# Optimization experiments

Measured on AMD Instinct MI355X. Metric: run time of the kernel, lower is better.

The kernel has to match this reference:

```python
import jax, jax.numpy as jnp
import numpy as np

V, D, T_BLK, H, HS = 50257, 512, 2048, 8, 64
B, T = 2, 2048


def setup_inputs() -> dict:
    key = jax.random.key(0)
    ks = jax.random.split(key, 12)
    s = 0.02
    return {
        "idx": jax.random.randint(ks[0], (B, T), 0, V),
        "targets": jax.random.randint(ks[1], (B, T), 0, V),
        "tok_emb": jax.random.normal(ks[2], (V, D), jnp.float32) * s,
        "pos_emb": jax.random.normal(ks[3], (T_BLK, D), jnp.float32) * s,
        "wq": jax.random.normal(ks[4], (H, D, HS), jnp.float32) * s,
        "wk": jax.random.normal(ks[5], (H, D, HS), jnp.float32) * s,
        "wv": jax.random.normal(ks[6], (H, D, HS), jnp.float32) * s,
        "w1": jax.random.normal(ks[7], (D, D), jnp.float32) * s,
        "b1": jnp.zeros((D,), jnp.float32),
        "w_head": jax.random.normal(ks[8], (D, V), jnp.float32) * s,
        "b_head": jnp.zeros((V,), jnp.float32),
    }


def _forward(idx, targets, tok_emb, pos_emb, wq, wk, wv, w1, b1, w_head, b_head):
    b, t = idx.shape
    x = tok_emb[idx] + pos_emb[:t]                        # [B,T,D]
    # batched per-head QKV (equivalent to the per-head Linear loop)
    q = jnp.einsum("btd,hde->bhte", x, wq)                # [B,H,T,hs]
    k = jnp.einsum("btd,hde->bhte", x, wk)
    v = jnp.einsum("btd,hde->bhte", x, wv)
    scores = jnp.einsum("bhte,bhse->bhts", q, k) / jnp.sqrt(jnp.float32(HS))
    causal = jnp.tril(jnp.ones((t, t), bool))
    scores = jnp.where(causal, scores, -jnp.inf)
    weights = jax.nn.softmax(scores, axis=-1)
    att = jnp.einsum("bhts,bhse->bhte", weights, v)       # [B,H,T,hs]
    att = att.transpose(0, 2, 1, 3).reshape(b, t, H * HS)  # head-concat order
    x_ff = jax.nn.relu(att @ w1 + b1)                      # [B,T,D]
    logits = x_ff @ w_head + b_head                        # [B,T,V]
    logp = jax.nn.log_softmax(logits, axis=-1)
    loss = -jnp.mean(jnp.take_along_axis(logp, targets[..., None], axis=-1))
    return logits, loss


def reference(idx, targets, tok_emb, pos_emb, wq, wk, wv, w1, b1, w_head, b_head):
    return _forward(idx, targets, tok_emb, pos_emb, wq, wk, wv, w1, b1, w_head, b_head)
```

## Files before the change

kernel.cpp:

```cpp
#include <hip/hip_runtime.h>
#include <hip/hip_bf16.h>
#include <stdint.h>

#define V_SZ   50257
#define NPAD   50432
#define NT_HEAD 197
#define D_SZ   512
#define HS_SZ  64
#define H_N    8
#define T_SZ   2048
#define ROWS   4096

typedef __bf16 bf16x8 __attribute__((ext_vector_type(8)));
typedef __bf16 bf16x4 __attribute__((ext_vector_type(4)));
typedef float  f32x4  __attribute__((ext_vector_type(4)));

__device__ __forceinline__ void gload_lds16(const void* g, void* l) {
  auto gp = (const __attribute__((address_space(1))) uint32_t*)(uintptr_t)g;
  auto lp = (__attribute__((address_space(3))) uint32_t*)(uintptr_t)l;
  __builtin_amdgcn_global_load_lds(gp, lp, 16, 0, 0);
}

__global__ __launch_bounds__(256) void k_embed(const int* __restrict__ idx,
    const float* __restrict__ tok, const float* __restrict__ pos,
    __bf16* __restrict__ xb) {
  const int row = blockIdx.x;
  const int tpos = row & (T_SZ - 1);
  const int tokid = idx[row];
  const int d = threadIdx.x * 2;
  float2 tv = *(const float2*)(tok + (size_t)tokid * D_SZ + d);
  float2 pv = *(const float2*)(pos + (size_t)tpos * D_SZ + d);
  __bf16* o = xb + (size_t)row * D_SZ + d;
  o[0] = (__bf16)(tv.x + pv.x);
  o[1] = (__bf16)(tv.y + pv.y);
}

__global__ __launch_bounds__(256) void k_prep_wqkv(const float* __restrict__ wq,
    const float* __restrict__ wk, const float* __restrict__ wv, __bf16* __restrict__ dst) {
  const int id = blockIdx.x * 256 + threadIdx.x;
  const int n = id >> 9, dd = id & 511;
  const int mi = n >> 9, rem = n & 511, h = rem >> 6, e = rem & 63;
  const float* src = (mi == 0) ? wq : ((mi == 1) ? wk : wv);
  dst[id] = (__bf16)src[((size_t)h * D_SZ + dd) * HS_SZ + e];
}

__global__ __launch_bounds__(256) void k_prep_w1(const float* __restrict__ w1,
                                                 __bf16* __restrict__ dst) {
  const int id = blockIdx.x * 256 + threadIdx.x;
  const int n = id >> 9, kk = id & 511;
  dst[id] = (__bf16)w1[(size_t)kk * D_SZ + n];
}

__global__ void k_prep_wh(const float* __restrict__ wh, __bf16* __restrict__ dst) {
  __shared__ float tile[32][33];
  const int n0 = blockIdx.x * 32, d0 = blockIdx.y * 32;
  const int tx = threadIdx.x, ty = threadIdx.y;
  #pragma unroll
  for (int i = 0; i < 4; ++i) {
    int dd = d0 + ty + i * 8, n = n0 + tx;
    tile[ty + i * 8][tx] = (n < V_SZ) ? wh[(size_t)dd * V_SZ + n] : 0.f;
  }
  __syncthreads();
  #pragma unroll
  for (int i = 0; i < 4; ++i) {
    int n = n0 + ty + i * 8, dd = d0 + tx;
    dst[(size_t)n * D_SZ + dd] = (__bf16)tile[tx][ty + i * 8];
  }
}

template <int EPI>
__global__ __launch_bounds__(256) void k_gemm(const __bf16* __restrict__ A,
    const __bf16* __restrict__ Bt, const float* __restrict__ bias,
    __bf16* __restrict__ outH, __bf16* __restrict__ outK, __bf16* __restrict__ outV) {
  __shared__ __bf16 As[128 * 32];
  __shared__ __bf16 Bs[128 * 32];
  const int t = threadIdx.x, lane = t & 63, w = t >> 6;
  const int wr = w >> 1, wc = w & 1;
  const int m0 = blockIdx.x * 128, n0 = blockIdx.y * 128;
  const int srow = lane >> 2, k8 = (lane & 3) * 8;

  f32x4 zero = {0.f, 0.f, 0.f, 0.f};
  f32x4 acc[4][4];
  #pragma unroll
  for (int mm = 0; mm < 4; ++mm)
    #pragma unroll
    for (int nn = 0; nn < 4; ++nn) acc[mm][nn] = zero;

  const __bf16* Ag = A  + (size_t)(m0 + w * 16 + srow) * D_SZ + k8;
  const __bf16* Bg = Bt + (size_t)(n0 + w * 16 + srow) * D_SZ + k8;
  char* AsB = (char*)As + w * 1024;
  char* BsB = (char*)Bs + w * 1024;
  const int kslot = (lane >> 4) * 8;
  const int arow = wr * 64 + (lane & 15);
  const int brow = wc * 64 + (lane & 15);

  for (int kt = 0; kt < 16; ++kt) {
    const int k0 = kt * 32;
    gload_lds16(Ag + k0,             AsB);
    gload_lds16(Ag + 64 * D_SZ + k0, AsB + 4096);
    gload_lds16(Bg + k0,             BsB);
    gload_lds16(Bg + 64 * D_SZ + k0, BsB + 4096);
    __syncthreads();

    bf16x8 af[4], bfr[4];
    #pragma unroll
    for (int mm = 0; mm < 4; ++mm)
      af[mm] = *(const bf16x8*)(As + (arow + mm * 16) * 32 + kslot);
    #pragma unroll
    for (int nn = 0; nn < 4; ++nn)
      bfr[nn] = *(const bf16x8*)(Bs + (brow + nn * 16) * 32 + kslot);
    #pragma unroll
    for (int mm = 0; mm < 4; ++mm)
      #pragma unroll
      for (int nn = 0; nn < 4; ++nn)
        acc[mm][nn] = __builtin_amdgcn_mfma_f32_16x16x32_bf16(af[mm], bfr[nn], acc[mm][nn], 0, 0, 0);
    __syncthreads();
  }

  const int lrow = (lane >> 4) * 4, lcol = lane & 15;
  #pragma unroll
  for (int mm = 0; mm < 4; ++mm) {
    #pragma unroll
    for (int nn = 0; nn < 4; ++nn) {
      const int grow0 = m0 + wr * 64 + mm * 16 + lrow;
      const int gcol  = n0 + wc * 64 + nn * 16 + lcol;
      if (EPI == 0) {
        const int mi = gcol >> 9, rem = gcol & 511, hh = rem >> 6, e = rem & 63;
        const int bb = grow0 >> 11, tt0 = grow0 & 2047;
        const int bhh = bb * H_N + hh;
        if (mi == 2) {
          bf16x4 pk = { (__bf16)acc[mm][nn][0], (__bf16)acc[mm][nn][1],
                        (__bf16)acc[mm][nn][2], (__bf16)acc[mm][nn][3] };
          *(bf16x4*)(outV + ((size_t)bhh * HS_SZ + e) * T_SZ + tt0) = pk;
        } else {
          __bf16* dq = (mi == 0 ? outH : outK) + ((size_t)bhh * T_SZ + tt0) * HS_SZ + e;
          const float sc = (mi == 0) ? 0.125f : 1.f;
          #pragma unroll
          for (int j = 0; j < 4; ++j) dq[(size_t)j * HS_SZ] = (__bf16)(acc[mm][nn][j] * sc);
        }
      } else {
        #pragma unroll
        for (int j = 0; j < 4; ++j) {
          float xv = acc[mm][nn][j] + bias[gcol];
          outH[(size_t)(grow0 + j) * D_SZ + gcol] = (__bf16)(xv > 0.f ? xv : 0.f);
        }
      }
    }
  }
}

__global__ __launch_bounds__(512, 2) void k_ghead(const __bf16* __restrict__ A,
    const __bf16* __restrict__ Bt, const float* __restrict__ bias,
    float* __restrict__ logits, float2* __restrict__ part) {
  __shared__ char lds[131072];
  const int t = threadIdx.x, lane = t & 63, w = t >> 6;
  const int wr = w >> 2, wc = w & 3;
  const int m0 = blockIdx.x * 256, n0 = blockIdx.y * 256;
  const int r8 = lane >> 3, cc = lane & 7;
  const int lm = lane & 15, g = lane >> 4, l7 = lane & 7;
  const int csw = (cc ^ r8) << 4;
  const int srow8 = w * 8 + r8;

  f32x4 acc[8][4];
  #pragma unroll
  for (int mm = 0; mm < 8; ++mm)
    #pragma unroll
    for (int nn = 0; nn < 4; ++nn) acc[mm][nn] = f32x4{0.f, 0.f, 0.f, 0.f};

  const char* Ab = (const char*)A  + (size_t)m0 * (D_SZ * 2);
  const char* Bb = (const char*)Bt + (size_t)n0 * (D_SZ * 2);

  auto STAGE = [&](int buf, int kt) {
    char* Al = lds + buf * 65536;
    char* Bl = Al + 32768;
    const char* Asrc = Ab + kt * 128;
    const char* Bsrc = Bb + kt * 128;
    #pragma unroll
    for (int i = 0; i < 4; ++i) {
      gload_lds16(Asrc + (size_t)(i * 64 + srow8) * 1024 + csw, Al + (i * 64 + w * 8) * 128);
      gload_lds16(Bsrc + (size_t)(i * 64 + srow8) * 1024 + csw, Bl + (i * 64 + w * 8) * 128);
    }
  };

  STAGE(0, 0);
  STAGE(1, 1);
  asm volatile("s_waitcnt vmcnt(8)" ::: "memory");
  __builtin_amdgcn_s_barrier();
  asm volatile("" ::: "memory");

  for (int kt = 0; kt < 8; ++kt) {
    const char* Al = lds + (kt & 1) * 65536;
    const char* Bl = Al + 32768;
    #pragma unroll
    for (int kh = 0; kh < 2; ++kh) {
      const int ch = ((g + kh * 4) ^ l7) << 4;
      bf16x8 a[8], b[4];
      #pragma unroll
      for (int mm = 0; mm < 8; ++mm)
        a[mm] = *(const bf16x8*)(Al + (wr * 128 + mm * 16 + lm) * 128 + ch);
      #pragma unroll
      for (int nn = 0; nn < 4; ++nn)
        b[nn] = *(const bf16x8*)(Bl + (wc * 64 + nn * 16 + lm) * 128 + ch);
      #pragma unroll
      for (int mm = 0; mm < 8; ++mm)
        #pragma unroll
        for (int nn = 0; nn < 4; ++nn)
          acc[mm][nn] = __builtin_amdgcn_mfma_f32_16x16x32_bf16(a[mm], b[nn], acc[mm][nn], 0, 0, 0);
    }
    if (kt == 7) break;
    __builtin_amdgcn_s_barrier();
    asm volatile("" ::: "memory");
    if (kt < 6) {
      STAGE(kt & 1, kt + 2);
      asm volatile("s_waitcnt vmcnt(8)" ::: "memory");
    } else {
      asm volatile("s_waitcnt vmcnt(0)" ::: "memory");
    }
    __builtin_amdgcn_s_barrier();
    asm volatile("" ::: "memory");
  }
  __syncthreads();

  float* tr   = (float*)lds;
  float* redS = tr + 32 * 260;
  const int colL = wc * 64 + lm;
  float bj[4]; int vok[4];
  #pragma unroll
  for (int nn = 0; nn < 4; ++nn) {
    const int gc = n0 + colL + nn * 16;
    vok[nn] = (gc < V_SZ);
    bj[nn] = vok[nn] ? bias[gc] : 0.f;
  }
  const int r32s = t >> 4, c16 = t & 15;
  #pragma unroll
  for (int mm = 0; mm < 8; ++mm) {
    if (mm) __syncthreads();
    float sj[4];
    #pragma unroll
    for (int j = 0; j < 4; ++j) {
      const int r32 = wr * 16 + g * 4 + j;
      float s = 0.f;
      #pragma unroll
      for (int nn = 0; nn < 4; ++nn) {
        const float v = acc[mm][nn][j] + bj[nn];
        tr[r32 * 260 + colL + nn * 16] = v;
        if (vok[nn]) s += __expf(v);
      }
      sj[j] = s;
    }
    #pragma unroll
    for (int j = 0; j < 4; ++j) {
      float s = sj[j];
      s += __shfl_xor(s, 1); s += __shfl_xor(s, 2);
      s += __shfl_xor(s, 4); s += __shfl_xor(s, 8);
      if (lm == 0) redS[(wr * 128 + mm * 16 + g * 4 + j) * 4 + wc] = s;
    }
    __syncthreads();
    const int grow = m0 + (r32s >> 4) * 128 + mm * 16 + (r32s & 15);
    float* gp = logits + (size_t)grow * V_SZ;
    #pragma unroll
    for (int i = 0; i < 4; ++i) {
      const int c4 = c16 + 16 * i;
      const int gc0 = n0 + c4 * 4;
      f32x4 vv = *(const f32x4*)(tr + r32s * 260 + c4 * 4);
      if (gc0 + 3 < V_SZ) {
        __builtin_nontemporal_store(vv, (f32x4*)(gp + gc0));
      } else {
        if (gc0     < V_SZ) __builtin_nontemporal_store(vv.x, gp + gc0);
        if (gc0 + 1 < V_SZ) __builtin_nontemporal_store(vv.y, gp + gc0 + 1);
        if (gc0 + 2 < V_SZ) __builtin_nontemporal_store(vv.z, gp + gc0 + 2);
        if (gc0 + 3 < V_SZ) __builtin_nontemporal_store(vv.w, gp + gc0 + 3);
      }
    }
  }
  __syncthreads();
  if (t < 256) {
    const float S = redS[t * 4] + redS[t * 4 + 1] + redS[t * 4 + 2] + redS[t * 4 + 3];
    part[(size_t)(m0 + t) * NT_HEAD + blockIdx.y] = float2{0.f, S};
  }
}

__global__ __launch_bounds__(256) void k_attn(const __bf16* __restrict__ qbf,
    const __bf16* __restrict__ kbf, const __bf16* __restrict__ vbf,
    __bf16* __restrict__ xatt) {
  const int qt = 31 - blockIdx.x;
  const int bh = blockIdx.y;
  const int b = bh >> 3, h = bh & 7;
  const int t = threadIdx.x, lane = t & 63, w = t >> 6;
  const int qr = lane & 15, g = lane >> 4, r7 = qr & 7;
  __shared__ __bf16 Klds[64 * 64];
  __shared__ __bf16 Vt[64 * 64];
  __shared__ __bf16 Plds[4][16 * 72];

  const int qglob = qt * 64 + w * 16 + qr;
  const __bf16* qrow_g = qbf + ((size_t)bh * T_SZ + qglob) * HS_SZ + g * 8;
  const bf16x8 qf0 = *(const bf16x8*)(qrow_g);
  const bf16x8 qf1 = *(const bf16x8*)(qrow_g + 32);

  f32x4 att[4];
  #pragma unroll
  for (int n = 0; n < 4; ++n) att[n] = f32x4{0.f, 0.f, 0.f, 0.f};
  float m = -3.0e38f, l = 0.f;

  const char* Kg = (const char*)(kbf + (size_t)bh * T_SZ * HS_SZ);
  const char* Vg = (const char*)(vbf + (size_t)bh * HS_SZ * T_SZ);
  const int r8 = lane >> 3, cc = lane & 7;
  const int csw = ((cc ^ r8) << 4);

  for (int kt = 0; kt <= qt; ++kt) {
    if (kt) __syncthreads();
    {
      const char* ks = Kg + (size_t)(kt * 64 + w * 16) * 128;
      gload_lds16(ks + r8 * 128 + csw,        (char*)Klds + w * 2048);
      gload_lds16(ks + 1024 + r8 * 128 + csw, (char*)Klds + w * 2048 + 1024);
      const char* vs = Vg + (size_t)(w * 16) * (T_SZ * 2) + kt * 128;
      gload_lds16(vs + r8 * (T_SZ * 2) + csw,                   (char*)Vt + w * 2048);
      gload_lds16(vs + (8 + r8) * (T_SZ * 2) + csw,             (char*)Vt + w * 2048 + 1024);
    }
    __syncthreads();

    const bool diag = (kt == qt);
    f32x4 acc[4];
    #pragma unroll
    for (int a = 0; a < 4; ++a) {
      if (diag && a > w) {
        acc[a] = f32x4{-3.0e38f, -3.0e38f, -3.0e38f, -3.0e38f};
      } else {
        const char* kb = (const char*)Klds + (a * 16 + qr) * 128;
        bf16x8 ka0 = *(const bf16x8*)(kb + ((g ^ r7) << 4));
        bf16x8 ka1 = *(const bf16x8*)(kb + (((g + 4) ^ r7) << 4));
        f32x4 z = {0.f, 0.f, 0.f, 0.f};
        z = __builtin_amdgcn_mfma_f32_16x16x32_bf16(ka0, qf0, z, 0, 0, 0);
        z = __builtin_amdgcn_mfma_f32_16x16x32_bf16(ka1, qf1, z, 0, 0, 0);
        acc[a] = z;
      }
    }
    if (diag) {
      #pragma unroll
      for (int a = 0; a < 4; ++a)
        #pragma unroll
        for (int j = 0; j < 4; ++j)
          if (a * 16 + g * 4 + j > w * 16 + qr) acc[a][j] = -3.0e38f;
    }

    float mloc = -3.0e38f;
    #pragma unroll
    for (int a = 0; a < 4; ++a)
      #pragma unroll
      for (int j = 0; j < 4; ++j) mloc = fmaxf(mloc, acc[a][j]);
    mloc = fmaxf(mloc, __shfl_xor(mloc, 16));
    mloc = fmaxf(mloc, __shfl_xor(mloc, 32));
    const float newm = fmaxf(m, mloc);
    const float alpha = __expf(m - newm);
    float lloc = 0.f;
    #pragma unroll
    for (int a = 0; a < 4; ++a) {
      float p0 = __expf(acc[a][0] - newm);
      float p1 = __expf(acc[a][1] - newm);
      float p2 = __expf(acc[a][2] - newm);
      float p3 = __expf(acc[a][3] - newm);
      lloc += (p0 + p1) + (p2 + p3);
      bf16x4 pw = { (__bf16)p0, (__bf16)p1, (__bf16)p2, (__bf16)p3 };
      *(bf16x4*)((char*)&Plds[w][0] + qr * 144 + (a * 16 + g * 4) * 2) = pw;
    }
    lloc += __shfl_xor(lloc, 16);
    lloc += __shfl_xor(lloc, 32);
    l = l * alpha + lloc;
    m = newm;

    #pragma unroll
    for (int j = 0; j < 4; ++j) {
      const float aj = __shfl(alpha, g * 4 + j);
      #pragma unroll
      for (int n = 0; n < 4; ++n) att[n][j] *= aj;
    }

    #pragma unroll
    for (int c = 0; c < 2; ++c) {
      bf16x8 pa = *(const bf16x8*)((const char*)&Plds[w][0] + qr * 144 + c * 64 + g * 16);
      #pragma unroll
      for (int n = 0; n < 4; ++n) {
        const int vrow = n * 16 + qr;
        bf16x8 vb = *(const bf16x8*)((const char*)Vt + vrow * 128 + (((c * 4 + g) ^ r7) << 4));
        att[n] = __builtin_amdgcn_mfma_f32_16x16x32_bf16(pa, vb, att[n], 0, 0, 0);
      }
    }
  }

  #pragma unroll
  for (int j = 0; j < 4; ++j) {
    const float lj = __shfl(l, g * 4 + j);
    const float inv = 1.f / lj;
    const int row = qt * 64 + w * 16 + g * 4 + j;
    __bf16* orow = xatt + ((size_t)(b * T_SZ + row)) * D_SZ + h * HS_SZ + qr;
    #pragma unroll
    for (int n = 0; n < 4; ++n) orow[n * 16] = (__bf16)(att[n][j] * inv);
  }
}

__global__ __launch_bounds__(256) void k_lsemerge(const float2* __restrict__ part,
                                                  float* __restrict__ lse) {
  const int row = blockIdx.x * 4 + (threadIdx.x >> 6);
  const int lane = threadIdx.x & 63;
  const float2* pr = part + (size_t)row * NT_HEAD;
  float M = -3.0e38f, S = 0.f;
  for (int i = lane; i < NT_HEAD; i += 64) {
    float2 p = pr[i];
    float nm = fmaxf(M, p.x);
    S = S * __expf(M - nm) + p.y * __expf(p.x - nm);
    M = nm;
  }
  #pragma unroll
  for (int off = 1; off < 64; off <<= 1) {
    float Mo = __shfl_xor(M, off), So = __shfl_xor(S, off);
    float nm = fmaxf(M, Mo);
    S = S * __expf(M - nm) + So * __expf(Mo - nm);
    M = nm;
  }
  if (lane == 0) lse[row] = M + __logf(S);
}

__global__ __launch_bounds__(256) void k_loss(const float* __restrict__ logits,
    const float* __restrict__ lse, const int* __restrict__ tgt,
    float* __restrict__ outloss) {
  float acc = 0.f;
  for (int r = threadIdx.x; r < ROWS; r += 256)
    acc += lse[r] - logits[(size_t)r * V_SZ + tgt[r]];
  #pragma unroll
  for (int off = 32; off > 0; off >>= 1) acc += __shfl_down(acc, off);
  __shared__ float pw[4];
  if ((threadIdx.x & 63) == 0) pw[threadIdx.x >> 6] = acc;
  __syncthreads();
  if (threadIdx.x == 0) outloss[0] = (pw[0] + pw[1] + pw[2] + pw[3]) * (1.f / ROWS);
}

extern "C" void kernel_launch(void* const* d_in, const int* in_sizes, int n_in,
                              void* d_out, int out_size, void* d_ws, size_t ws_size,
                              hipStream_t stream) {
  const int*   idx = (const int*)d_in[0];
  const int*   tgt = (const int*)d_in[1];
  const float* tok = (const float*)d_in[2];
  const float* pos = (const float*)d_in[3];
  const float* wq  = (const float*)d_in[4];
  const float* wk  = (const float*)d_in[5];
  const float* wv  = (const float*)d_in[6];
  const float* w1  = (const float*)d_in[7];
  const float* b1  = (const float*)d_in[8];
  const float* wh  = (const float*)d_in[9];
  const float* bh  = (const float*)d_in[10];

  float* logits = (float*)d_out;
  float* lossp  = logits + (size_t)ROWS * V_SZ;

  char* ws = (char*)d_ws;
  __bf16* xb   = (__bf16*)(ws + 0);
  __bf16* Bqkv = (__bf16*)(ws + (4u  << 20));
  __bf16* B1t  = (__bf16*)(ws + (11u << 19));
  __bf16* qbf  = (__bf16*)(ws + (6u  << 20));
  __bf16* kbf  = (__bf16*)(ws + (10u << 20));
  __bf16* vbf  = (__bf16*)(ws + (14u << 20));
  float2* part = (float2*)(ws + 0);
  float*  lse  = (float*) (ws + (20u << 20));
  __bf16* xatt = (__bf16*)(ws + (30u << 20));
  __bf16* Aff  = (__bf16*)(ws + (34u << 20));
  __bf16* Wht  = (__bf16*)(ws + (38u << 20));

  k_embed    <<<ROWS, 256, 0, stream>>>(idx, tok, pos, xb);
  k_prep_wqkv<<<3072, 256, 0, stream>>>(wq, wk, wv, Bqkv);
  k_prep_w1  <<<1024, 256, 0, stream>>>(w1, B1t);
  k_prep_wh  <<<dim3(NPAD / 32, 16), dim3(32, 8), 0, stream>>>(wh, Wht);

  k_gemm<0><<<dim3(32, 12),  256, 0, stream>>>(xb,   Bqkv, nullptr, qbf, kbf, vbf);
  k_attn   <<<dim3(32, 16),  256, 0, stream>>>(qbf, kbf, vbf, xatt);
  k_gemm<1><<<dim3(32, 4),   256, 0, stream>>>(xatt, B1t,  b1,  Aff, nullptr, nullptr);
  k_ghead  <<<dim3(16, NT_HEAD), 512, 0, stream>>>(Aff, Wht, bh, logits, part);

  k_lsemerge<<<ROWS / 4, 256, 0, stream>>>(part, lse);
  k_loss    <<<1,        256, 0, stream>>>(logits, lse, tgt, lossp);
}
```

Measured before the change: 567.7 us.

## Shrink head GEMM N-tile to 128 and use triple-buffered split-stage pipeline

The LM-head GEMM block tile narrows from 256x256 to 256x128, which roughly doubles the number of column tiles, shrinks the padding of the vocab dimension, and halves the accumulators per thread. The K loop moves from double to triple buffering. Global-to-LDS loads for the stage two steps ahead are split into two halves, each interleaved with one K-half of MFMA work, and the MFMA bursts run at raised wave priority via s_setprio. The aim is better overlap of memory and compute and better load balance across CUs, at the cost of loading the A tile twice as often and using more LDS per block.

```diff
diff --git a/kernel.cpp b/kernel.cpp
--- a/kernel.cpp
+++ b/kernel.cpp
@@ -3,8 +3,8 @@
 #include <stdint.h>
 
 #define V_SZ   50257
-#define NPAD   50432
-#define NT_HEAD 197
+#define NPAD   50304
+#define NT_HEAD 393
 #define D_SZ   512
 #define HS_SZ  64
 #define H_N    8
@@ -152,82 +152,98 @@
 __global__ __launch_bounds__(512, 2) void k_ghead(const __bf16* __restrict__ A,
     const __bf16* __restrict__ Bt, const float* __restrict__ bias,
     float* __restrict__ logits, float2* __restrict__ part) {
-  __shared__ char lds[131072];
+  __shared__ char lds[147456];
   const int t = threadIdx.x, lane = t & 63, w = t >> 6;
   const int wr = w >> 2, wc = w & 3;
-  const int m0 = blockIdx.x * 256, n0 = blockIdx.y * 256;
+  const int m0 = blockIdx.x * 256, n0 = blockIdx.y * 128;
   const int r8 = lane >> 3, cc = lane & 7;
   const int lm = lane & 15, g = lane >> 4, l7 = lane & 7;
   const int csw = (cc ^ r8) << 4;
   const int srow8 = w * 8 + r8;
 
-  f32x4 acc[8][4];
+  f32x4 acc[8][2];
   #pragma unroll
   for (int mm = 0; mm < 8; ++mm)
     #pragma unroll
-    for (int nn = 0; nn < 4; ++nn) acc[mm][nn] = f32x4{0.f, 0.f, 0.f, 0.f};
+    for (int nn = 0; nn < 2; ++nn) acc[mm][nn] = f32x4{0.f, 0.f, 0.f, 0.f};
 
   const char* Ab = (const char*)A  + (size_t)m0 * (D_SZ * 2);
   const char* Bb = (const char*)Bt + (size_t)n0 * (D_SZ * 2);
 
-  auto STAGE = [&](int buf, int kt) {
-    char* Al = lds + buf * 65536;
-    char* Bl = Al + 32768;
-    const char* Asrc = Ab + kt * 128;
-    const char* Bsrc = Bb + kt * 128;
-    #pragma unroll
-    for (int i = 0; i < 4; ++i) {
-      gload_lds16(Asrc + (size_t)(i * 64 + srow8) * 1024 + csw, Al + (i * 64 + w * 8) * 128);
-      gload_lds16(Bsrc + (size_t)(i * 64 + srow8) * 1024 + csw, Bl + (i * 64 + w * 8) * 128);
-    }
+  auto stageA = [&](int buf, int kt, int c) {
+    gload_lds16(Ab + (size_t)(c * 64 + srow8) * 1024 + kt * 128 + csw,
+                lds + buf * 49152 + (c * 64 + w * 8) * 128);
   };
-
-  STAGE(0, 0);
-  STAGE(1, 1);
-  asm volatile("s_waitcnt vmcnt(8)" ::: "memory");
+  auto stageB = [&](int buf, int kt, int c) {
+    gload_lds16(Bb + (size_t)(c * 64 + srow8) * 1024 + kt * 128 + csw,
+                lds + buf * 49152 + 32768 + (c * 64 + w * 8) * 128);
+  };
+
+  #pragma unroll
+  for (int c = 0; c < 4; ++c) stageA(0, 0, c);
+  stageB(0, 0, 0); stageB(0, 0, 1);
+  #pragma unroll
+  for (int c = 0; c < 4; ++c) stageA(1, 1, c);
+  stageB(1, 1, 0); stageB(1, 1, 1);
+  asm volatile("s_waitcnt vmcnt(6)" ::: "memory");
   __builtin_amdgcn_s_barrier();
-  asm volatile("" ::: "memory");
-
+
+  #pragma unroll
   for (int kt = 0; kt < 8; ++kt) {
-    const char* Al = lds + (kt & 1) * 65536;
+    const int bi = kt % 3, bs = (kt + 2) % 3;
+    const char* Al = lds + bi * 49152;
     const char* Bl = Al + 32768;
-    #pragma unroll
-    for (int kh = 0; kh < 2; ++kh) {
-      const int ch = ((g + kh * 4) ^ l7) << 4;
-      bf16x8 a[8], b[4];
+    if (kt < 6) { stageA(bs, kt + 2, 0); stageA(bs, kt + 2, 1); stageA(bs, kt + 2, 2); }
+    {
+      bf16x8 a[8], b[2];
       #pragma unroll
       for (int mm = 0; mm < 8; ++mm)
-        a[mm] = *(const bf16x8*)(Al + (wr * 128 + mm * 16 + lm) * 128 + ch);
-      #pragma unroll
-      for (int nn = 0; nn < 4; ++nn)
-        b[nn] = *(const bf16x8*)(Bl + (wc * 64 + nn * 16 + lm) * 128 + ch);
+        a[mm] = *(const bf16x8*)(Al + (wr * 128 + mm * 16 + lm) * 128 + ((g ^ l7) << 4));
+      #pragma unroll
+      for (int nn = 0; nn < 2; ++nn)
+        b[nn] = *(const bf16x8*)(Bl + (wc * 32 + nn * 16 + lm) * 128 + ((g ^ l7) << 4));
+      __builtin_amdgcn_s_barrier();
+      asm volatile("s_waitcnt lgkmcnt(0)" ::: "memory");
+      __builtin_amdgcn_s_setprio(1);
       #pragma unroll
       for (int mm = 0; mm < 8; ++mm)
         #pragma unroll
-        for (int nn = 0; nn < 4; ++nn)
+        for (int nn = 0; nn < 2; ++nn)
           acc[mm][nn] = __builtin_amdgcn_mfma_f32_16x16x32_bf16(a[mm], b[nn], acc[mm][nn], 0, 0, 0);
-    }
-    if (kt == 7) break;
-    __builtin_amdgcn_s_barrier();
-    asm volatile("" ::: "memory");
-    if (kt < 6) {
-      STAGE(kt & 1, kt + 2);
-      asm volatile("s_waitcnt vmcnt(8)" ::: "memory");
-    } else {
-      asm volatile("s_waitcnt vmcnt(0)" ::: "memory");
-    }
-    __builtin_amdgcn_s_barrier();
-    asm volatile("" ::: "memory");
+      __builtin_amdgcn_s_setprio(0);
+      __builtin_amdgcn_s_barrier();
+    }
+    if (kt < 6) { stageA(bs, kt + 2, 3); stageB(bs, kt + 2, 0); stageB(bs, kt + 2, 1); }
+    {
+      bf16x8 a[8], b[2];
+      #pragma unroll
+      for (int mm = 0; mm < 8; ++mm)
+        a[mm] = *(const bf16x8*)(Al + (wr * 128 + mm * 16 + lm) * 128 + (((4 + g) ^ l7) << 4));
+      #pragma unroll
+      for (int nn = 0; nn < 2; ++nn)
+        b[nn] = *(const bf16x8*)(Bl + (wc * 32 + nn * 16 + lm) * 128 + (((4 + g) ^ l7) << 4));
+      __builtin_amdgcn_s_barrier();
+      asm volatile("s_waitcnt lgkmcnt(0)" ::: "memory");
+      __builtin_amdgcn_s_setprio(1);
+      #pragma unroll
+      for (int mm = 0; mm < 8; ++mm)
+        #pragma unroll
+        for (int nn = 0; nn < 2; ++nn)
+          acc[mm][nn] = __builtin_amdgcn_mfma_f32_16x16x32_bf16(a[mm], b[nn], acc[mm][nn], 0, 0, 0);
+      __builtin_amdgcn_s_setprio(0);
+      if (kt < 6)       { asm volatile("s_waitcnt vmcnt(6)" ::: "memory"); }
+      else if (kt == 6) { asm volatile("s_waitcnt vmcnt(0)" ::: "memory"); }
+      __builtin_amdgcn_s_barrier();
+    }
   }
   __syncthreads();
 
   float* tr   = (float*)lds;
-  float* redS = tr + 32 * 260;
-  const int colL = wc * 64 + lm;
-  float bj[4]; int vok[4];
-  #pragma unroll
-  for (int nn = 0; nn < 4; ++nn) {
-    const int gc = n0 + colL + nn * 16;
+  float* redS = tr + 32 * 132;
+  float bj[2]; int vok[2];
+  #pragma unroll
+  for (int nn = 0; nn < 2; ++nn) {
+    const int gc = n0 + wc * 32 + nn * 16 + lm;
     vok[nn] = (gc < V_SZ);
     bj[nn] = vok[nn] ? bias[gc] : 0.f;
   }
@@ -241,9 +257,9 @@
       const int r32 = wr * 16 + g * 4 + j;
       float s = 0.f;
       #pragma unroll
-      for (int nn = 0; nn < 4; ++nn) {
+      for (int nn = 0; nn < 2; ++nn) {
         const float v = acc[mm][nn][j] + bj[nn];
-        tr[r32 * 260 + colL + nn * 16] = v;
+        tr[r32 * 132 + wc * 32 + nn * 16 + lm] = v;
         if (vok[nn]) s += __expf(v);
       }
       sj[j] = s;
@@ -259,10 +275,10 @@
     const int grow = m0 + (r32s >> 4) * 128 + mm * 16 + (r32s & 15);
     float* gp = logits + (size_t)grow * V_SZ;
     #pragma unroll
-    for (int i = 0; i < 4; ++i) {
+    for (int i = 0; i < 2; ++i) {
       const int c4 = c16 + 16 * i;
       const int gc0 = n0 + c4 * 4;
-      f32x4 vv = *(const f32x4*)(tr + r32s * 260 + c4 * 4);
+      f32x4 vv = *(const f32x4*)(tr + r32s * 132 + c4 * 4);
       if (gc0 + 3 < V_SZ) {
         __builtin_nontemporal_store(vv, (f32x4*)(gp + gc0));
       } else {
```

New measurement: 605.5 us. 6.6% more time.
